# Optimization experiments

Hardware: AMD Instinct MI355X
Metric: run time of the kernel (lower is better)

The kernel has to match this reference:

```python
import jax, jax.numpy as jnp
import numpy as np
import math

B, C, H, WIN = 8, 96, 224, 7
D_STATE, DT_RANK = 16, 6
PERK = C // 4
K_RATIO = 0.25


def nearest_perfect_square(val):
    if val <= 0:
        return 0
    s = math.sqrt(val)
    lo = math.floor(s) ** 2
    hi = math.ceil(s) ** 2
    return lo if abs(lo - val) <= abs(hi - val) else hi


def setup_inputs() -> dict:
    key = jax.random.key(0)
    ks = jax.random.split(key, 8)
    x = jax.random.normal(ks[0], (B, C, H, H), dtype=jnp.float32)
    router_w1 = jax.random.normal(ks[1], (C // 4, C), jnp.float32) * (1.0 / math.sqrt(C))
    router_b1 = jnp.zeros((C // 4,), jnp.float32)
    router_w2 = jax.random.normal(ks[2], (1, C // 4), jnp.float32) * (1.0 / math.sqrt(C // 4))
    router_b2 = jnp.zeros((1,), jnp.float32)
    x_proj_weight = jax.random.normal(ks[3], (4, DT_RANK + 2 * D_STATE, PERK), jnp.float32) * (1.0 / math.sqrt(PERK))
    std = DT_RANK ** -0.5
    dt_projs_weight = jax.random.uniform(ks[4], (4, PERK, DT_RANK), jnp.float32, -std, std)
    dt = jnp.exp(jax.random.uniform(ks[5], (4, PERK), jnp.float32) * (math.log(0.1) - math.log(0.001)) + math.log(0.001))
    dt = jnp.clip(dt, 1e-4)
    dt_projs_bias = dt + jnp.log(-jnp.expm1(-dt))  # inv-softplus init as in dt_init_fn
    A_logs = jnp.log(jnp.tile(jnp.arange(1, D_STATE + 1, dtype=jnp.float32)[None, :], (4 * PERK, 1)))
    Ds = jnp.ones((4 * PERK,), jnp.float32)
    return {"x": x, "router_w1": router_w1, "router_b1": router_b1, "router_w2": router_w2,
            "router_b2": router_b2, "x_proj_weight": x_proj_weight, "dt_projs_weight": dt_projs_weight,
            "dt_projs_bias": dt_projs_bias, "A_logs": A_logs, "Ds": Ds}


def reference(x, router_w1, router_b1, router_w2, router_b2, x_proj_weight,
              dt_projs_weight, dt_projs_bias, A_logs, Ds):
    Bb, Cc, Hh, Ww = x.shape
    nH = Hh // WIN
    N = nH * nH
    # window partition: b c (nh p1) (nw p2) -> b (nh nw) c p1 p2
    windows = x.reshape(Bb, Cc, nH, WIN, nH, WIN).transpose(0, 2, 4, 1, 3, 5).reshape(Bb, N, Cc, WIN, WIN)
    # router scores
    pooled = windows.mean(axis=(-2, -1))  # [B,N,C]
    hid = jax.nn.gelu(pooled @ router_w1.T + router_b1, approximate=False)
    logits = (hid @ router_w2.T + router_b2)[..., 0]  # [B,N]
    probs = jax.nn.softmax(logits, axis=1)
    top_k = min(max(nearest_perfect_square(N * K_RATIO), 1), N)
    n = int(math.isqrt(top_k))
    rw, sel = jax.lax.top_k(probs, top_k)  # sorted descending, like torch.topk
    windows_flat = windows.reshape(Bb, N, -1)
    cur = jnp.take_along_axis(windows_flat, sel[:, :, None], axis=1)  # [B,topk,C*w*w]
    cur = cur.reshape(Bb, n, n, Cc, WIN, WIN)
    L = n * n * WIN * WIN
    # channel interleave (p k) -> (k p), k=4
    x_int = cur.reshape(Bb, n, n, Cc // 4, 4, WIN, WIN).transpose(0, 1, 2, 4, 3, 5, 6)  # [B,n,n,4,perK,w,w]

    def local_scan(w, column_first, flip):
        # w: [B,n,n,D,wh,ww] -> [B,D,L]
        if column_first:
            w = w.transpose(0, 3, 2, 1, 5, 4)
        else:
            w = w.transpose(0, 3, 1, 2, 4, 5)
        w = w.reshape(Bb, -1, L)
        if flip:
            w = w[..., ::-1]
        return w

    xs = jnp.stack([
        local_scan(x_int[:, :, :, 0], False, False),
        local_scan(x_int[:, :, :, 1], True, False),
        local_scan(x_int[:, :, :, 2], False, True),
        local_scan(x_int[:, :, :, 3], True, True),
    ], axis=1)  # [B,4,perK,L]

    x_dbl = jnp.einsum('bkdl,kcd->bkcl', xs, x_proj_weight)
    dts = x_dbl[:, :, :DT_RANK]
    Bmat = x_dbl[:, :, DT_RANK:DT_RANK + D_STATE]  # [B,4,Nst,L]
    Cmat = x_dbl[:, :, DT_RANK + D_STATE:]
    dts = jnp.einsum('bkrl,kdr->bkdl', dts, dt_projs_weight)  # [B,4,perK,L]
    A_g = -jnp.exp(A_logs).reshape(4, PERK, D_STATE)
    delta = jax.nn.softplus(dts + dt_projs_bias.reshape(4, PERK)[None, :, :, None])

    # selective scan (grouped): h_{l} = exp(delta*A)*h_{l-1} + delta*u*B_l ; y_l = <h_l, C_l>
    dl = jnp.moveaxis(delta, -1, 0)  # [L,B,4,perK]
    ul = jnp.moveaxis(xs, -1, 0)
    Bl = jnp.moveaxis(Bmat, -1, 0)   # [L,B,4,Nst]
    Cl = jnp.moveaxis(Cmat, -1, 0)
    h0 = jnp.zeros((Bb, 4, PERK, D_STATE), jnp.float32)

    def step(h, inp):
        d, u, Bt, Ct = inp
        h = jnp.exp(d[..., None] * A_g) * h + (d * u)[..., None] * Bt[:, :, None, :]
        return h, jnp.einsum('bkdn,bkn->bkd', h, Ct)

    _, ys = jax.lax.scan(step, h0, (dl, ul, Bl, Cl))
    y = jnp.moveaxis(ys, 0, -1) + xs * Ds.reshape(4, PERK)[None, :, :, None]  # [B,4,perK,L]

    def local_reverse(yk, column_first, flip):
        if flip:
            yk = yk[..., ::-1]
        if column_first:
            yk = yk.reshape(Bb, -1, n, n, WIN, WIN).transpose(0, 1, 3, 5, 2, 4).reshape(Bb, -1, L)
        else:
            yk = yk.reshape(Bb, -1, n, n, WIN, WIN).transpose(0, 1, 2, 4, 3, 5).reshape(Bb, -1, L)
        return yk

    yout = jnp.concatenate([
        local_reverse(y[:, 0], False, False),
        local_reverse(y[:, 1], True, False),
        local_reverse(y[:, 2], False, True),
        local_reverse(y[:, 3], True, True),
    ], axis=1)  # [B,C,L]
    yout = yout.reshape(Bb, Cc, n * n, WIN * WIN).transpose(0, 2, 1, 3).reshape(Bb, top_k, -1)
    cur_out = yout * rw[:, :, None]
    residual = windows_flat * probs[:, :, None]
    residual = residual.at[jnp.arange(Bb)[:, None], sel].set(cur_out)
    new = windows_flat + residual
    return new.reshape(Bb, Cc, -1)
```

## Files before the change

kernel.cpp:

```cpp
#include <hip/hip_runtime.h>
#include <math.h>

#define BBATCH 8
#define CC 96
#define HH 224
#define NHW 32
#define NWIN 1024
#define TOPK 256
#define PERK 24
#define DST 16
#define DTR 6
#define LL 12544
#define LCP 52
#define NG 13
#define TCH 256
#define NBK 32
#define XROW 1248
#define WST4 2080
#define LOG2E 1.4426950408889634f

#define EXP2F(x) __builtin_amdgcn_exp2f(x)

#define OFF_POOL 0
#define OFF_LOG  786432
#define OFF_PROB 794624
#define OFF_RW   802816
#define OFF_RANK 804864
#define OFF_SEL  813056
#define OFF_WEFF 815104
#define OFF_CP   820480
#define OFF_CS   3966208
#define OFF_XSD  7111936
#define OFF_STG  17335552

#define ROR_ADD(v, CTRL) \
    v += __int_as_float(__builtin_amdgcn_update_dpp(0, __float_as_int(v), CTRL, 0xf, 0xf, true))

__device__ __forceinline__ unsigned f2b(float f) {
    unsigned u = __float_as_uint(f);
    return (u + 0x7fffu + ((u >> 16) & 1u)) >> 16;
}
__device__ __forceinline__ unsigned pk(float a, float b) {
    return f2b(a) | (f2b(b) << 16);
}
__device__ __forceinline__ float lo_f(unsigned w) { return __uint_as_float(w << 16); }
__device__ __forceinline__ float hi_f(unsigned w) { return __uint_as_float(w & 0xffff0000u); }

__global__ void k_pool(const float* __restrict__ x, float* __restrict__ pooled) {
    int bc = blockIdx.x;
    const float* xp = x + (size_t)bc * HH * HH;
    float* pp = pooled + (size_t)bc * NWIN;
    for (int w = threadIdx.x; w < NWIN; w += blockDim.x) {
        int wr = w >> 5, wc = w & 31;
        const float* base = xp + (wr * 7) * HH + wc * 7;
        float s = 0.f;
        #pragma unroll
        for (int i = 0; i < 7; ++i) {
            #pragma unroll
            for (int j = 0; j < 7; ++j) s += base[i * HH + j];
        }
        pp[w] = s * (1.0f / 49.0f);
    }
}

__global__ __launch_bounds__(64) void k_router(
        const float* __restrict__ pooled,
        const float* __restrict__ w1, const float* __restrict__ b1,
        const float* __restrict__ w2, const float* __restrict__ b2,
        const float* __restrict__ xpw, const float* __restrict__ dtw,
        float* __restrict__ wcomb, float* __restrict__ logits) {
    __shared__ float sw1[PERK * CC];
    __shared__ float sb1[PERK];
    __shared__ float sw2[PERK];
    int b = blockIdx.x >> 4, slice = blockIdx.x & 15;
    int tid = threadIdx.x;
    for (int i = blockIdx.x * 64 + tid; i < 4 * 56 * PERK; i += 128 * 64) {
        int k = i / (56 * PERK), rem = i - k * (56 * PERK);
        int row = rem / PERK, c = rem - row * PERK;
        float v;
        if (row < PERK) {
            v = 0.f;
            #pragma unroll
            for (int r = 0; r < DTR; ++r)
                v += dtw[(k * PERK + row) * DTR + r] * xpw[(k * 38 + r) * PERK + c];
        } else {
            v = xpw[(k * 38 + (row - PERK + DTR)) * PERK + c];
        }
        wcomb[i] = v;
    }
    for (int i = tid; i < PERK * CC; i += 64) sw1[i] = w1[i];
    if (tid < PERK) { sb1[tid] = b1[tid]; sw2[tid] = w2[tid]; }
    __syncthreads();
    int w = slice * 64 + tid;
    float hid[PERK];
    #pragma unroll
    for (int j = 0; j < PERK; ++j) hid[j] = sb1[j];
    const float* pp = pooled + (size_t)b * CC * NWIN + w;
    for (int c = 0; c < CC; ++c) {
        float pv = pp[(size_t)c * NWIN];
        #pragma unroll
        for (int j = 0; j < PERK; ++j) hid[j] += pv * sw1[j * CC + c];
    }
    float lg = b2[0];
    #pragma unroll
    for (int j = 0; j < PERK; ++j) {
        float hv = hid[j];
        float g = 0.5f * hv * (1.0f + erff(hv * 0.7071067811865476f));
        lg += g * sw2[j];
    }
    logits[b * NWIN + w] = lg;
}

__global__ __launch_bounds__(64) void k_rankF(const float* __restrict__ logits,
        float* __restrict__ probs, float* __restrict__ rw,
        int* __restrict__ rank, int* __restrict__ sel) {
    __shared__ __attribute__((aligned(16))) float sp[NWIN];
    __shared__ float red[64];
    int b = blockIdx.x >> 4, slice = blockIdx.x & 15;
    int tid = threadIdx.x;
    for (int i = tid; i < NWIN / 4; i += 64)
        ((float4*)sp)[i] = ((const float4*)(logits + (size_t)b * NWIN))[i];
    __syncthreads();
    float m = -1e30f;
    for (int i = tid; i < NWIN; i += 64) m = fmaxf(m, sp[i]);
    red[tid] = m; __syncthreads();
    for (int o = 32; o > 0; o >>= 1) { if (tid < o) red[tid] = fmaxf(red[tid], red[tid + o]); __syncthreads(); }
    float mx = red[0]; __syncthreads();
    for (int i = tid; i < NWIN; i += 64) sp[i] = expf(sp[i] - mx);
    __syncthreads();
    float s = 0.f;
    for (int i = tid; i < NWIN; i += 64) s += sp[i];
    red[tid] = s; __syncthreads();
    for (int o = 32; o > 0; o >>= 1) { if (tid < o) red[tid] += red[tid + o]; __syncthreads(); }
    float sum = red[0]; __syncthreads();
    for (int i = tid; i < NWIN; i += 64) sp[i] = sp[i] / sum;
    __syncthreads();
    int w = slice * 64 + tid;
    float p = sp[w];
    probs[b * NWIN + w] = p;
    int r = 0;
    for (int j = 0; j < NWIN; j += 4) {
        float4 pj = *(const float4*)&sp[j];
        r += (int)((pj.x > p) || (pj.x == p && (j + 0) < w));
        r += (int)((pj.y > p) || (pj.y == p && (j + 1) < w));
        r += (int)((pj.z > p) || (pj.z == p && (j + 2) < w));
        r += (int)((pj.w > p) || (pj.w == p && (j + 3) < w));
    }
    rank[b * NWIN + w] = r;
    if (r < TOPK) { sel[b * TOPK + r] = w; rw[b * TOPK + r] = p; }
}

__device__ __forceinline__ float softplus_f(float v) {
    return fmaxf(v, 0.f) + __logf(1.0f + __expf(-fabsf(v)));
}

__device__ __forceinline__ int window_wsel(const int* sel, int b, int k, int t) {
    int qscan = (k >= 2) ? (255 - t) : t;
    int selidx = (k & 1) ? (((qscan & 15) << 4) | (qscan >> 4)) : qscan;
    return sel[b * TOPK + selidx];
}

__global__ __launch_bounds__(256) void k_gather(const float* __restrict__ x,
        const int* __restrict__ sel, float* __restrict__ xsd) {
    const int total = NBK * TCH * XROW;
    for (int e = blockIdx.x * 256 + threadIdx.x; e < total; e += gridDim.x * 256) {
        int blk = e / XROW;
        int rem = e - blk * XROW;
        int d2 = rem / LCP, j = rem - d2 * LCP;
        float v = 0.f;
        if (j < 49) {
            int t = blk & 255, bk = blk >> 8, k = bk & 3, b = bk >> 2;
            int wsel = window_wsel(sel, b, k, t);
            int pix = (k >= 2) ? 48 - j : j;
            int q7 = pix / 7, r7 = pix - q7 * 7;
            int wi = (k & 1) ? r7 : q7;
            int wj = (k & 1) ? q7 : r7;
            v = x[(((size_t)b * CC + 4 * d2 + k) * HH + (wsel >> 5) * 7 + wi) * HH
                  + (wsel & 31) * 7 + wj];
        }
        xsd[e] = v;
    }
}

__global__ __launch_bounds__(384, 4) void k_prodT(
        const float* __restrict__ xsd, const float* __restrict__ wcomb,
        const float* __restrict__ dtb, const float* __restrict__ alogs,
        float* __restrict__ stage, float* __restrict__ carrP, float* __restrict__ carrS) {
    __shared__ __attribute__((aligned(16))) float sxs[PERK][LCP];
    __shared__ __attribute__((aligned(16))) float sprj[56][LCP];
    __shared__ float swt[56 * PERK];
    __shared__ float sbias[PERK];
    int blk = blockIdx.x; int k = (blk >> 8) & 3;
    int tid = threadIdx.x;
    const float4* xin = (const float4*)(xsd + (size_t)blk * XROW);
    for (int i = tid; i < XROW / 4; i += 384) ((float4*)sxs)[i] = xin[i];
    for (int i = tid; i < 56 * PERK; i += 384) swt[i] = wcomb[k * (56 * PERK) + i];
    if (tid < PERK) sbias[tid] = dtb[k * PERK + tid];
    if (tid < 168) { int r = tid / 3, j = 49 + tid % 3; sprj[r][j] = 0.f; }
    __syncthreads();
    if (tid < 28 * NG) {
        int rp = tid / NG, g = tid - rp * NG; int j = g * 4;
        int row0 = rp * 2, row1 = row0 + 1;
        bool isdl = (row0 < PERK);
        float bs0 = isdl ? sbias[row0] : 0.f;
        float bs1 = isdl ? sbias[row1] : 0.f;
        float a0x = bs0, a0y = bs0, a0z = bs0, a0w = bs0;
        float a1x = bs1, a1y = bs1, a1z = bs1, a1w = bs1;
        #pragma unroll
        for (int d2 = 0; d2 < PERK; ++d2) {
            float w0 = swt[row0 * PERK + d2];
            float w1 = swt[row1 * PERK + d2];
            float4 v = *(const float4*)&sxs[d2][j];
            a0x += w0 * v.x; a0y += w0 * v.y; a0z += w0 * v.z; a0w += w0 * v.w;
            a1x += w1 * v.x; a1y += w1 * v.y; a1z += w1 * v.z; a1w += w1 * v.w;
        }
        if (isdl) {
            a0x = softplus_f(a0x); a0y = softplus_f(a0y); a0z = softplus_f(a0z); a0w = softplus_f(a0w);
            a1x = softplus_f(a1x); a1y = softplus_f(a1y); a1z = softplus_f(a1z); a1w = softplus_f(a1w);
        }
        if (g < 12) {
            float4 o0 = {a0x, a0y, a0z, a0w}; *(float4*)&sprj[row0][j] = o0;
            float4 o1 = {a1x, a1y, a1z, a1w}; *(float4*)&sprj[row1][j] = o1;
        } else {
            sprj[row0][j] = a0x; sprj[row1][j] = a1x;
        }
    }
    __syncthreads();
    uint4* sgP = (uint4*)(stage + (size_t)blk * WST4);
    uint4* sgQ = sgP + 312;
    for (int tsk = tid; tsk < 312; tsk += 384) {
        int g4 = tsk / 24, d2 = tsk - g4 * 24; int j = g4 * 4;
        uint4 o;
        o.x = pk(sprj[d2][j + 0], sxs[d2][j + 0]);
        o.y = pk(sprj[d2][j + 1], sxs[d2][j + 1]);
        o.z = pk(sprj[d2][j + 2], sxs[d2][j + 2]);
        o.w = pk(sprj[d2][j + 3], sxs[d2][j + 3]);
        sgP[tsk] = o;
    }
    for (int tsk = tid; tsk < 208; tsk += 384) {
        int g4 = tsk / 16, s2 = tsk - g4 * 16; int j = g4 * 4;
        uint4 o;
        o.x = pk(sprj[24 + s2][j + 0], sprj[40 + s2][j + 0]);
        o.y = pk(sprj[24 + s2][j + 1], sprj[40 + s2][j + 1]);
        o.z = pk(sprj[24 + s2][j + 2], sprj[40 + s2][j + 2]);
        o.w = pk(sprj[24 + s2][j + 3], sprj[40 + s2][j + 3]);
        sgQ[tsk] = o;
    }
    int d = tid >> 4, s = tid & 15;
    float A2 = -__expf(alogs[(k * PERK + d) * DST + s]) * LOG2E;
    float P = 1.f, S = 0.f;
    for (int g = 0; g < NG; ++g) {
        int j = g * 4;
        float4 dl4 = *(const float4*)&sprj[d][j];
        float4 xs4 = *(const float4*)&sxs[d][j];
        float4 B4  = *(const float4*)&sprj[24 + s][j];
        float aa;
        aa = EXP2F(dl4.x * A2); S = aa * S + (dl4.x * xs4.x) * B4.x; P *= aa;
        aa = EXP2F(dl4.y * A2); S = aa * S + (dl4.y * xs4.y) * B4.y; P *= aa;
        aa = EXP2F(dl4.z * A2); S = aa * S + (dl4.z * xs4.z) * B4.z; P *= aa;
        aa = EXP2F(dl4.w * A2); S = aa * S + (dl4.w * xs4.w) * B4.w; P *= aa;
    }
    size_t cidx = (size_t)blk * 384 + tid;
    carrP[cidx] = P; carrS[cidx] = S;
}

__global__ __launch_bounds__(256) void k_cb(const float* carrP, const float* carrS,
        float* hin, const float* __restrict__ x, const float* __restrict__ probs,
        const int* __restrict__ rank, float* __restrict__ out) {
    if (blockIdx.x < 48) {
        int gid = blockIdx.x * 256 + threadIdx.x;
        int bk = gid / 384, ds = gid - bk * 384;
        float Hv = 0.f;
        for (int t = 0; t < TCH; ++t) {
            size_t idx = ((size_t)bk * TCH + t) * 384 + ds;
            float pv = carrP[idx], sv = carrS[idx];
            hin[idx] = Hv;
            Hv = pv * Hv + sv;
        }
        return;
    }
    int bid = blockIdx.x - 48;
    int wr = bid % NHW; int bc = bid / NHW;
    int b = bc / CC;
    __shared__ float buf[7 * HH];
    __shared__ float fmul[NHW];
    __shared__ int   fsel[NHW];
    int tid = threadIdx.x;
    const float* xp = x + ((size_t)bc * HH + wr * 7) * HH;
    for (int i = tid; i < 7 * HH; i += 256) buf[i] = xp[i];
    if (tid < NHW) {
        int w = wr * NHW + tid;
        fsel[tid] = (rank[b * NWIN + w] < TOPK);
        fmul[tid] = 1.0f + probs[b * NWIN + w];
    }
    __syncthreads();
    int c = bc - b * CC;
    for (int idx = tid; idx < NHW * 49; idx += 256) {
        int wc = idx / 49, r = idx - wc * 49;
        if (fsel[wc]) continue;
        int ri = r / 7, rj = r - ri * 7;
        float v = buf[ri * HH + wc * 7 + rj];
        int w = wr * NHW + wc;
        out[(((size_t)b * NWIN + w) * CC + c) * 49 + r] = v * fmul[wc];
    }
}

#define BST(hv, widx, pw, qw, jj)                                                  \
    {                                                                              \
        float dl_ = lo_f(pw), xs_ = hi_f(pw), Bv_ = lo_f(qw), Cv_ = hi_f(qw);      \
        float aa_ = EXP2F(dl_ * A2);                                               \
        hv = aa_ * hv + (dl_ * xs_) * Bv_;                                         \
        float part_ = hv * Cv_;                                                    \
        ROR_ADD(part_, 0x121); ROR_ADD(part_, 0x122);                              \
        ROR_ADD(part_, 0x124); ROR_ADD(part_, 0x128);                              \
        if (s == 0 && (jj) < 49) sy[widx][d][jj] = part_ + xs_ * Dsr;              \
    }

__global__ __launch_bounds__(384, 4) void k_scanT(
        const float* __restrict__ alogs, const float* __restrict__ dsv,
        const float* __restrict__ hin, const float* __restrict__ stage,
        float* __restrict__ xsd) {
    __shared__ __attribute__((aligned(16))) float sy[2][PERK][LCP];
    int blk2 = blockIdx.x;
    int w0 = blk2 * 2, w1 = w0 + 1;
    int k = (w0 >> 8) & 3;
    int tid = threadIdx.x;
    int d = tid >> 4, s = tid & 15;
    float A2 = -__expf(alogs[(k * PERK + d) * DST + s]) * LOG2E;
    float Dsr = dsv[k * PERK + d];
    float h0 = hin[(size_t)w0 * 384 + tid];
    float h1 = hin[(size_t)w1 * 384 + tid];
    const uint4* pP0 = (const uint4*)(stage + (size_t)w0 * WST4) + d;
    const uint4* pQ0 = (const uint4*)(stage + (size_t)w0 * WST4) + 312 + s;
    const uint4* pP1 = (const uint4*)(stage + (size_t)w1 * WST4) + d;
    const uint4* pQ1 = (const uint4*)(stage + (size_t)w1 * WST4) + 312 + s;
    uint4 P0c = pP0[0],  Q0c = pQ0[0],  P1c = pP1[0],  Q1c = pQ1[0];
    uint4 P0n = pP0[24], Q0n = pQ0[16], P1n = pP1[24], Q1n = pQ1[16];
    for (int g4 = 0; g4 < NG; ++g4) {
        uint4 a0 = P0c, b0 = Q0c, a1 = P1c, b1 = Q1c;
        P0c = P0n; Q0c = Q0n; P1c = P1n; Q1c = Q1n;
        if (g4 + 2 < NG) {
            int jP = (g4 + 2) * 24, jQ = (g4 + 2) * 16;
            P0n = pP0[jP]; Q0n = pQ0[jQ]; P1n = pP1[jP]; Q1n = pQ1[jQ];
        }
        int j = g4 * 4;
        BST(h0, 0, a0.x, b0.x, j);     BST(h1, 1, a1.x, b1.x, j);
        BST(h0, 0, a0.y, b0.y, j + 1); BST(h1, 1, a1.y, b1.y, j + 1);
        BST(h0, 0, a0.z, b0.z, j + 2); BST(h1, 1, a1.z, b1.z, j + 2);
        BST(h0, 0, a0.w, b0.w, j + 3); BST(h1, 1, a1.w, b1.w, j + 3);
    }
    __syncthreads();
    float* y0 = xsd + (size_t)w0 * XROW;
    float* y1 = xsd + (size_t)w1 * XROW;
    for (int idx = tid; idx < PERK * 49; idx += 384) {
        int j = idx / PERK, d2 = idx - j * PERK;
        y0[idx] = sy[0][d2][j];
        y1[idx] = sy[1][d2][j];
    }
}

__global__ __launch_bounds__(256) void k_yadd(const float* __restrict__ ysrc,
        const float* __restrict__ x, const int* __restrict__ sel,
        const float* __restrict__ rw, float* __restrict__ out) {
    __shared__ float ytile[CC * 49];
    int qo = blockIdx.x & 255; int b = blockIdx.x >> 8;
    int wsel = sel[b * TOPK + qo];
    float p = rw[b * TOPK + qo];
    for (int idx = threadIdx.x; idx < CC * 49; idx += 256) {
        int k = idx / 1176; int r1 = idx - k * 1176;
        int u = r1 / 168;   int r2 = r1 - u * 168;
        int wj = r2 / 24;   int d = r2 - wj * 24;
        int rest = qo * 7 + u;
        int b2 = rest & 15; int aw = rest >> 4;
        int wi = aw % 7;    int a = aw / 7;
        int q   = (k & 1) ? (b2 * 16 + a) : (a * 16 + b2);
        int pix = (k & 1) ? (wj * 7 + wi) : (wi * 7 + wj);
        int uu = q * 49 + pix;
        int l = (k >= 2) ? (LL - 1 - uu) : uu;
        int bk = b * 4 + k;
        int t2 = l / 49, jj = l - t2 * 49;
        ytile[(k * PERK + d) * 49 + u * 7 + wj] =
            p * ysrc[((size_t)(bk * 256 + t2)) * XROW + jj * PERK + d];
    }
    __syncthreads();
    float* ob = out + ((size_t)(b * NWIN + wsel) * CC) * 49;
    int gi0 = (wsel >> 5) * 7, gj0 = (wsel & 31) * 7;
    for (int e = threadIdx.x; e < CC * 49; e += 256) {
        int C = e / 49, cell = e - C * 49;
        int u = cell / 7, wj = cell - u * 7;
        float xv = x[(((size_t)b * CC + C) * HH + gi0 + u) * HH + gj0 + wj];
        ob[e] = xv + ytile[e];
    }
}

extern "C" void kernel_launch(void* const* d_in, const int* in_sizes, int n_in,
                              void* d_out, int out_size, void* d_ws, size_t ws_size,
                              hipStream_t stream) {
    const float* x   = (const float*)d_in[0];
    const float* w1  = (const float*)d_in[1];
    const float* b1  = (const float*)d_in[2];
    const float* w2  = (const float*)d_in[3];
    const float* b2  = (const float*)d_in[4];
    const float* xpw = (const float*)d_in[5];
    const float* dtw = (const float*)d_in[6];
    const float* dtb = (const float*)d_in[7];
    const float* alg = (const float*)d_in[8];
    const float* dsv = (const float*)d_in[9];
    float* out = (float*)d_out;
    float* ws  = (float*)d_ws;

    float* pooled = ws + OFF_POOL;
    float* logits = ws + OFF_LOG;
    float* probs  = ws + OFF_PROB;
    float* rwv    = ws + OFF_RW;
    int*   rank   = (int*)(ws + OFF_RANK);
    int*   sel    = (int*)(ws + OFF_SEL);
    float* wcomb  = ws + OFF_WEFF;
    float* cP  = ws + OFF_CP;
    float* cS  = ws + OFF_CS;
    float* xsd = ws + OFF_XSD;
    float* stage = ws + OFF_STG;

    k_pool  <<<BBATCH * CC, 256, 0, stream>>>(x, pooled);
    k_router<<<BBATCH * 16, 64, 0, stream>>>(pooled, w1, b1, w2, b2, xpw, dtw, wcomb, logits);
    k_rankF <<<BBATCH * 16, 64, 0, stream>>>(logits, probs, rwv, rank, sel);
    k_gather<<<2048, 256, 0, stream>>>(x, sel, xsd);
    k_prodT <<<NBK * TCH, 384, 0, stream>>>(xsd, wcomb, dtb, alg, stage, cP, cS);
    k_cb    <<<48 + BBATCH * CC * NHW, 256, 0, stream>>>(cP, cS, cP, x, probs, rank, out);
    k_scanT <<<NBK * TCH / 2, 384, 0, stream>>>(alg, dsv, cP, stage, xsd);
    k_yadd  <<<BBATCH * TOPK, 256, 0, stream>>>(xsd, x, sel, rwv, out);
}
```

Measured before the change: 426.6 us.

## Move unselected-window output write into final per-window output kernel

The unselected-window residual write (x*(1+prob)) is taken out of the carry-scan kernel and merged into the final output kernel, which now launches one block per window and branches on the window's rank. The carry-propagation kernel becomes a standalone 48-block launch. Previously those two jobs shared a launch so their work could overlap. Now the serial carry chain runs alone, and the residual write lands after the scan instead of alongside it.

```diff
diff --git a/kernel.cpp b/kernel.cpp
--- a/kernel.cpp
+++ b/kernel.cpp
@@ -264,44 +264,15 @@
     carrP[cidx] = P; carrS[cidx] = S;
 }
 
-__global__ __launch_bounds__(256) void k_cb(const float* carrP, const float* carrS,
-        float* hin, const float* __restrict__ x, const float* __restrict__ probs,
-        const int* __restrict__ rank, float* __restrict__ out) {
-    if (blockIdx.x < 48) {
-        int gid = blockIdx.x * 256 + threadIdx.x;
-        int bk = gid / 384, ds = gid - bk * 384;
-        float Hv = 0.f;
-        for (int t = 0; t < TCH; ++t) {
-            size_t idx = ((size_t)bk * TCH + t) * 384 + ds;
-            float pv = carrP[idx], sv = carrS[idx];
-            hin[idx] = Hv;
-            Hv = pv * Hv + sv;
-        }
-        return;
-    }
-    int bid = blockIdx.x - 48;
-    int wr = bid % NHW; int bc = bid / NHW;
-    int b = bc / CC;
-    __shared__ float buf[7 * HH];
-    __shared__ float fmul[NHW];
-    __shared__ int   fsel[NHW];
-    int tid = threadIdx.x;
-    const float* xp = x + ((size_t)bc * HH + wr * 7) * HH;
-    for (int i = tid; i < 7 * HH; i += 256) buf[i] = xp[i];
-    if (tid < NHW) {
-        int w = wr * NHW + tid;
-        fsel[tid] = (rank[b * NWIN + w] < TOPK);
-        fmul[tid] = 1.0f + probs[b * NWIN + w];
-    }
-    __syncthreads();
-    int c = bc - b * CC;
-    for (int idx = tid; idx < NHW * 49; idx += 256) {
-        int wc = idx / 49, r = idx - wc * 49;
-        if (fsel[wc]) continue;
-        int ri = r / 7, rj = r - ri * 7;
-        float v = buf[ri * HH + wc * 7 + rj];
-        int w = wr * NHW + wc;
-        out[(((size_t)b * NWIN + w) * CC + c) * 49 + r] = v * fmul[wc];
+__global__ void k_carry(const float* carrP, const float* carrS, float* hin) {
+    int gid = blockIdx.x * blockDim.x + threadIdx.x;
+    int bk = gid / 384, ds = gid - bk * 384;
+    float Hv = 0.f;
+    for (int t = 0; t < TCH; ++t) {
+        size_t idx = ((size_t)bk * TCH + t) * 384 + ds;
+        float pv = carrP[idx], sv = carrS[idx];
+        hin[idx] = Hv;
+        Hv = pv * Hv + sv;
     }
 }
 
@@ -359,37 +330,50 @@
     }
 }
 
-__global__ __launch_bounds__(256) void k_yadd(const float* __restrict__ ysrc,
-        const float* __restrict__ x, const int* __restrict__ sel,
-        const float* __restrict__ rw, float* __restrict__ out) {
+__global__ __launch_bounds__(256) void k_out(const float* __restrict__ ysrc,
+        const float* __restrict__ x, const int* __restrict__ rank,
+        const float* __restrict__ probs, const float* __restrict__ rw,
+        float* __restrict__ out) {
     __shared__ float ytile[CC * 49];
-    int qo = blockIdx.x & 255; int b = blockIdx.x >> 8;
-    int wsel = sel[b * TOPK + qo];
-    float p = rw[b * TOPK + qo];
-    for (int idx = threadIdx.x; idx < CC * 49; idx += 256) {
-        int k = idx / 1176; int r1 = idx - k * 1176;
-        int u = r1 / 168;   int r2 = r1 - u * 168;
-        int wj = r2 / 24;   int d = r2 - wj * 24;
-        int rest = qo * 7 + u;
-        int b2 = rest & 15; int aw = rest >> 4;
-        int wi = aw % 7;    int a = aw / 7;
-        int q   = (k & 1) ? (b2 * 16 + a) : (a * 16 + b2);
-        int pix = (k & 1) ? (wj * 7 + wi) : (wi * 7 + wj);
-        int uu = q * 49 + pix;
-        int l = (k >= 2) ? (LL - 1 - uu) : uu;
-        int bk = b * 4 + k;
-        int t2 = l / 49, jj = l - t2 * 49;
-        ytile[(k * PERK + d) * 49 + u * 7 + wj] =
-            p * ysrc[((size_t)(bk * 256 + t2)) * XROW + jj * PERK + d];
-    }
-    __syncthreads();
-    float* ob = out + ((size_t)(b * NWIN + wsel) * CC) * 49;
-    int gi0 = (wsel >> 5) * 7, gj0 = (wsel & 31) * 7;
-    for (int e = threadIdx.x; e < CC * 49; e += 256) {
-        int C = e / 49, cell = e - C * 49;
-        int u = cell / 7, wj = cell - u * 7;
-        float xv = x[(((size_t)b * CC + C) * HH + gi0 + u) * HH + gj0 + wj];
-        ob[e] = xv + ytile[e];
+    int w = blockIdx.x & 1023; int b = blockIdx.x >> 10;
+    int r = rank[b * NWIN + w];
+    int tid = threadIdx.x;
+    float* ob = out + ((size_t)(b * NWIN + w) * CC) * 49;
+    int gi0 = (w >> 5) * 7, gj0 = (w & 31) * 7;
+    if (r < TOPK) {
+        int qo = r;
+        float p = rw[b * TOPK + qo];
+        for (int idx = tid; idx < CC * 49; idx += 256) {
+            int k = idx / 1176; int r1 = idx - k * 1176;
+            int u = r1 / 168;   int r2 = r1 - u * 168;
+            int wj = r2 / 24;   int d = r2 - wj * 24;
+            int rest = qo * 7 + u;
+            int b2 = rest & 15; int aw = rest >> 4;
+            int wi = aw % 7;    int a = aw / 7;
+            int q   = (k & 1) ? (b2 * 16 + a) : (a * 16 + b2);
+            int pix = (k & 1) ? (wj * 7 + wi) : (wi * 7 + wj);
+            int uu = q * 49 + pix;
+            int l = (k >= 2) ? (LL - 1 - uu) : uu;
+            int bk = b * 4 + k;
+            int t2 = l / 49, jj = l - t2 * 49;
+            ytile[(k * PERK + d) * 49 + u * 7 + wj] =
+                p * ysrc[((size_t)(bk * 256 + t2)) * XROW + jj * PERK + d];
+        }
+        __syncthreads();
+        for (int e = tid; e < CC * 49; e += 256) {
+            int C = e / 49, cell = e - C * 49;
+            int u = cell / 7, wj = cell - u * 7;
+            float xv = x[(((size_t)b * CC + C) * HH + gi0 + u) * HH + gj0 + wj];
+            ob[e] = xv + ytile[e];
+        }
+    } else {
+        float f = 1.0f + probs[b * NWIN + w];
+        for (int e = tid; e < CC * 49; e += 256) {
+            int C = e / 49, cell = e - C * 49;
+            int u = cell / 7, wj = cell - u * 7;
+            float xv = x[(((size_t)b * CC + C) * HH + gi0 + u) * HH + gj0 + wj];
+            ob[e] = xv * f;
+        }
     }
 }
 
@@ -426,7 +410,7 @@
     k_rankF <<<BBATCH * 16, 64, 0, stream>>>(logits, probs, rwv, rank, sel);
     k_gather<<<2048, 256, 0, stream>>>(x, sel, xsd);
     k_prodT <<<NBK * TCH, 384, 0, stream>>>(xsd, wcomb, dtb, alg, stage, cP, cS);
-    k_cb    <<<48 + BBATCH * CC * NHW, 256, 0, stream>>>(cP, cS, cP, x, probs, rank, out);
+    k_carry <<<48, 256, 0, stream>>>(cP, cS, cP);
     k_scanT <<<NBK * TCH / 2, 384, 0, stream>>>(alg, dsv, cP, stage, xsd);
-    k_yadd  <<<BBATCH * TOPK, 256, 0, stream>>>(xsd, x, sel, rwv, out);
-}
+    k_out   <<<BBATCH * NWIN, 256, 0, stream>>>(xsd, x, rank, probs, rwv, out);
+}
```

Result: slower. 492.4 us (+15.4%).
